# Kernel tuning notes

Measured on AMD Instinct MI355X. Metric: run time of the kernel, lower is better.

The kernel has to match this reference:

```python
import jax, jax.numpy as jnp
import numpy as np

B, T, H = 4, 2048, 1024
DFF = 4 * H
MAX_DEPTH = 4
TARGET_DEPTH = 2.5
BUDGET_WEIGHT = 0.01
ACT_TAU = 0.99


def setup_inputs() -> dict:
    key = jax.random.key(0)
    ks = jax.random.split(key, 6)
    s = 0.02
    return {
        "x": jax.random.normal(ks[0], (B, T, H), dtype=jnp.float32),
        "Wb1": jax.random.normal(ks[1], (H, DFF), dtype=jnp.float32) * s,
        "bb1": jnp.zeros((DFF,), dtype=jnp.float32),
        "Wb2": jax.random.normal(ks[2], (DFF, H), dtype=jnp.float32) * s,
        "bb2": jnp.zeros((H,), dtype=jnp.float32),
        "Rw1": jax.random.normal(ks[3], (MAX_DEPTH - 1, H + 1, H // 2), dtype=jnp.float32) * s,
        "Rb1": jnp.zeros((MAX_DEPTH - 1, H // 2), dtype=jnp.float32),
        "Rw2": jax.random.normal(ks[4], (MAX_DEPTH - 1, H // 2, 1), dtype=jnp.float32) * s,
        "Rb2": jnp.zeros((MAX_DEPTH - 1, 1), dtype=jnp.float32),
    }


def _body(x, Wb1, bb1, Wb2, bb2):
    # transformer-style FFN body, exact (erf) GELU to match torch nn.GELU
    h = jax.nn.gelu(jnp.einsum("btd,df->btf", x, Wb1) + bb1, approximate=False)
    return jnp.einsum("btf,fd->btd", h, Wb2) + bb2


def reference(x, Wb1, bb1, Wb2, bb2, Rw1, Rb1, Rw2, Rb2):
    # mandatory first pass
    x = _body(x, Wb1, bb1, Wb2, bb2)
    lead = x.shape[:-1]  # (B, T)
    weight_sum = jnp.ones(lead, dtype=x.dtype)
    cumulative_p = jnp.zeros(lead, dtype=x.dtype)
    still_running = jnp.ones(lead, dtype=x.dtype)
    for i in range(MAX_DEPTH - 1):
        # router: concat spike-rate feature (zeros: no scalar aux from body)
        feat = jnp.concatenate([x, jnp.zeros(lead + (1,), dtype=x.dtype)], axis=-1)
        h = jax.nn.gelu(jnp.einsum("btf,fm->btm", feat, Rw1[i]) + Rb1[i], approximate=False)
        logit = (jnp.einsum("btm,mo->bto", h, Rw2[i]) + Rb2[i])[..., 0]
        p = jax.nn.sigmoid(logit)
        # ACT remainder trick
        remainder = jnp.clip(1.0 - cumulative_p, 0.0)
        would_halt = cumulative_p + p >= ACT_TAU
        weight = jnp.where(would_halt, remainder, p) * still_running
        # soft depth mix
        x_new = _body(x, Wb1, bb1, Wb2, bb2)
        w = weight[..., None]
        x = w * x_new + (1.0 - w) * x
        weight_sum = weight_sum + weight
        cumulative_p = cumulative_p + weight
        still_running = still_running * (~would_halt).astype(x.dtype)
    avg_depth = weight_sum.mean()
    budget_loss = BUDGET_WEIGHT * jnp.square(jax.nn.relu(avg_depth - TARGET_DEPTH))
    return x, budget_loss
```

## Files before the change

kernel.cpp:

```cpp
#include <hip/hip_runtime.h>
#include <hip/hip_bf16.h>
#include <math.h>

typedef __bf16 bf16_t;
typedef __attribute__((ext_vector_type(8))) __bf16 bf16x8;
typedef __attribute__((ext_vector_type(4))) __bf16 bf16x4;
typedef __attribute__((ext_vector_type(4))) float f32x4;

#define NTOK 8192
#define HDIM 1024
#define DFF  4096
#define RHID 512

__device__ __forceinline__ float gelu_exact(float v) {
  return 0.5f * v * (1.0f + erff(v * 0.70710678118654752f));
}

__device__ __forceinline__ void async_cp16(void* lds, const void* g) {
  __builtin_amdgcn_global_load_lds(
      (__attribute__((address_space(1))) void*)g,
      (__attribute__((address_space(3))) void*)lds, 16, 0, 0);
}

__device__ __forceinline__ void remap_tile(int g, int& mt, int& nt) {
  mt = ((g & 7) << 3) | ((g >> 3) & 7);
  nt = g >> 6;
}

template<int MODE>
__device__ __forceinline__ void body_tile(
    int mt, int nt,
    const bf16_t* __restrict__ A, const bf16_t* __restrict__ Bt,
    const float* __restrict__ bias, int N, int K,
    bf16_t* __restrict__ Hout, float* __restrict__ Xout,
    bf16_t* __restrict__ Xb, bf16_t* __restrict__ Xlo,
    const float* __restrict__ Wmix,
    bf16_t* As, bf16_t* Bs)
{
  const int tid  = threadIdx.x;
  const int lane = tid & 63;
  const int wv   = tid >> 6;
  const int wm   = wv >> 1;
  const int wn   = wv & 1;
  const int lr   = lane & 15;
  const int quad = lane >> 4;
  const int m0 = mt * 128;
  const int n0 = nt * 128;

  f32x4 acc[4][4];
#pragma unroll
  for (int i = 0; i < 4; ++i)
#pragma unroll
    for (int j = 0; j < 4; ++j)
      acc[i][j] = (f32x4){0.f, 0.f, 0.f, 0.f};

  const int c0 = tid;
  const int c1 = tid + 256;
  const int r0 = c0 >> 2, r1 = c1 >> 2;
  const int ks0 = ((c0 ^ r0) & 3) * 8;
  const int ks1 = ((c1 ^ r1) & 3) * 8;
  const bf16_t* Ag0 = A  + (size_t)(m0 + r0) * K + ks0;
  const bf16_t* Ag1 = A  + (size_t)(m0 + r1) * K + ks1;
  const bf16_t* Bg0 = Bt + (size_t)(n0 + r0) * K + ks0;
  const bf16_t* Bg1 = Bt + (size_t)(n0 + r1) * K + ks1;
  char* lA0 = (char*)As + c0 * 16;
  char* lA1 = (char*)As + c1 * 16;
  char* lB0 = (char*)Bs + c0 * 16;
  char* lB1 = (char*)Bs + c1 * 16;

  const int sw = ((quad ^ lr) & 3) * 8;

  for (int k0 = 0; k0 < K; k0 += 32) {
    __syncthreads();
    async_cp16(lA0, Ag0 + k0);
    async_cp16(lA1, Ag1 + k0);
    async_cp16(lB0, Bg0 + k0);
    async_cp16(lB1, Bg1 + k0);
    __syncthreads();
    bf16x8 af[4], bfr[4];
#pragma unroll
    for (int i = 0; i < 4; ++i)
      af[i] = *(const bf16x8*)&As[(wm * 64 + i * 16 + lr) * 32 + sw];
#pragma unroll
    for (int j = 0; j < 4; ++j)
      bfr[j] = *(const bf16x8*)&Bs[(wn * 64 + j * 16 + lr) * 32 + sw];
#pragma unroll
    for (int i = 0; i < 4; ++i)
#pragma unroll
      for (int j = 0; j < 4; ++j)
        acc[i][j] = __builtin_amdgcn_mfma_f32_16x16x32_bf16(af[i], bfr[j], acc[i][j], 0, 0, 0);
  }

#pragma unroll
  for (int i = 0; i < 4; ++i) {
#pragma unroll
    for (int r = 0; r < 4; ++r) {
      const int gm = m0 + wm * 64 + i * 16 + quad * 4 + r;
      float wmix = 0.f, onemw = 0.f;
      if (MODE == 2) { wmix = Wmix[gm]; onemw = 1.f - wmix; }
#pragma unroll
      for (int j = 0; j < 4; ++j) {
        const int gn = n0 + wn * 64 + j * 16 + lr;
        float v = acc[i][j][r] + bias[gn];
        if (MODE == 0) {
          Hout[(size_t)gm * N + gn] = (bf16_t)gelu_exact(v);
        } else {
          const size_t idx = (size_t)gm * N + gn;
          if (MODE == 2) v = wmix * v + onemw * Xout[idx];
          Xout[idx] = v;
          bf16_t hi = (bf16_t)v;
          Xb[idx]  = hi;
          Xlo[idx] = (bf16_t)(v - (float)hi);
        }
      }
    }
  }
}

__device__ __forceinline__ void router_tile(
    int mt, int nt,
    const bf16_t* __restrict__ Ah, const bf16_t* __restrict__ Al,
    const bf16_t* __restrict__ Bh, const bf16_t* __restrict__ Bl,
    const float* __restrict__ bias, float* __restrict__ Hr,
    bf16_t* Ahs, bf16_t* Als, bf16_t* Bhs, bf16_t* Bls)
{
  const int K = HDIM, N = RHID;
  const int tid  = threadIdx.x;
  const int lane = tid & 63;
  const int wv   = tid >> 6;
  const int wm   = wv >> 1;
  const int wn   = wv & 1;
  const int lr   = lane & 15;
  const int quad = lane >> 4;
  const int m0 = mt * 128;
  const int n0 = nt * 128;

  f32x4 acc[4][4];
#pragma unroll
  for (int i = 0; i < 4; ++i)
#pragma unroll
    for (int j = 0; j < 4; ++j)
      acc[i][j] = (f32x4){0.f, 0.f, 0.f, 0.f};

  const int c0 = tid;
  const int c1 = tid + 256;
  const int r0 = c0 >> 2, r1 = c1 >> 2;
  const int ks0 = ((c0 ^ r0) & 3) * 8;
  const int ks1 = ((c1 ^ r1) & 3) * 8;
  const size_t aoff0 = (size_t)(m0 + r0) * K + ks0;
  const size_t aoff1 = (size_t)(m0 + r1) * K + ks1;
  const size_t boff0 = (size_t)(n0 + r0) * K + ks0;
  const size_t boff1 = (size_t)(n0 + r1) * K + ks1;
  const int sw = ((quad ^ lr) & 3) * 8;

  for (int k0 = 0; k0 < K; k0 += 32) {
    __syncthreads();
    async_cp16((char*)Ahs + c0 * 16, Ah + aoff0 + k0);
    async_cp16((char*)Ahs + c1 * 16, Ah + aoff1 + k0);
    async_cp16((char*)Als + c0 * 16, Al + aoff0 + k0);
    async_cp16((char*)Als + c1 * 16, Al + aoff1 + k0);
    async_cp16((char*)Bhs + c0 * 16, Bh + boff0 + k0);
    async_cp16((char*)Bhs + c1 * 16, Bh + boff1 + k0);
    async_cp16((char*)Bls + c0 * 16, Bl + boff0 + k0);
    async_cp16((char*)Bls + c1 * 16, Bl + boff1 + k0);
    __syncthreads();
    bf16x8 ah[4], al[4], bh[4], bl[4];
#pragma unroll
    for (int i = 0; i < 4; ++i) {
      const int ao = (wm * 64 + i * 16 + lr) * 32 + sw;
      ah[i] = *(const bf16x8*)&Ahs[ao];
      al[i] = *(const bf16x8*)&Als[ao];
    }
#pragma unroll
    for (int j = 0; j < 4; ++j) {
      const int bo = (wn * 64 + j * 16 + lr) * 32 + sw;
      bh[j] = *(const bf16x8*)&Bhs[bo];
      bl[j] = *(const bf16x8*)&Bls[bo];
    }
#pragma unroll
    for (int i = 0; i < 4; ++i)
#pragma unroll
      for (int j = 0; j < 4; ++j) {
        acc[i][j] = __builtin_amdgcn_mfma_f32_16x16x32_bf16(ah[i], bh[j], acc[i][j], 0, 0, 0);
        acc[i][j] = __builtin_amdgcn_mfma_f32_16x16x32_bf16(al[i], bh[j], acc[i][j], 0, 0, 0);
        acc[i][j] = __builtin_amdgcn_mfma_f32_16x16x32_bf16(ah[i], bl[j], acc[i][j], 0, 0, 0);
      }
  }

#pragma unroll
  for (int i = 0; i < 4; ++i)
#pragma unroll
    for (int r = 0; r < 4; ++r) {
      const int gm = m0 + wm * 64 + i * 16 + quad * 4 + r;
#pragma unroll
      for (int j = 0; j < 4; ++j) {
        const int gn = n0 + wn * 64 + j * 16 + lr;
        Hr[(size_t)gm * N + gn] = gelu_exact(acc[i][j][r] + bias[gn]);
      }
    }
}

template<int MODE>
__global__ __launch_bounds__(256, 2)
void k_gemm(const bf16_t* __restrict__ A, const bf16_t* __restrict__ Bt,
            const float* __restrict__ bias, int N, int K,
            float* __restrict__ Xout, bf16_t* __restrict__ Xb,
            bf16_t* __restrict__ Xlo, const float* __restrict__ Wmix)
{
  __shared__ __align__(16) bf16_t sm[2 * 128 * 32];
  int mt, nt;
  remap_tile(blockIdx.x, mt, nt);
  body_tile<MODE>(mt, nt, A, Bt, bias, N, K, nullptr, Xout, Xb, Xlo, Wmix,
                  sm, sm + 128 * 32);
}

__global__ __launch_bounds__(256, 2)
void k_body0_router(const bf16_t* __restrict__ xb, const bf16_t* __restrict__ W1t,
                    const float* __restrict__ bb1, bf16_t* __restrict__ hbuf,
                    const bf16_t* __restrict__ xlo,
                    const bf16_t* __restrict__ R1h, const bf16_t* __restrict__ R1l,
                    const float* __restrict__ Rb1, float* __restrict__ hr,
                    int nbody)
{
  __shared__ __align__(16) bf16_t sm[4 * 128 * 32];
  const int g = blockIdx.x;
  if (g < nbody) {
    int mt, nt;
    remap_tile(g, mt, nt);
    body_tile<0>(mt, nt, xb, W1t, bb1, DFF, HDIM, hbuf,
                 nullptr, nullptr, nullptr, nullptr, sm, sm + 128 * 32);
  } else {
    int mt, nt;
    remap_tile(g - nbody, mt, nt);
    router_tile(mt, nt, xb, xlo, R1h, R1l, Rb1, hr,
                sm, sm + 128 * 32, sm + 2 * 128 * 32, sm + 3 * 128 * 32);
  }
}

__global__ void act_kernel(const float* __restrict__ Hr,
                           const float* __restrict__ rw2, const float* __restrict__ rb2,
                           float* __restrict__ cum_p, float* __restrict__ still_r,
                           float* __restrict__ wsum, float* __restrict__ wvec)
{
  const int t = blockIdx.x * 4 + (threadIdx.x >> 6);
  const int lane = threadIdx.x & 63;
  float s = 0.f;
#pragma unroll
  for (int j = 0; j < 8; ++j) {
    const int m = lane + j * 64;
    s += Hr[(size_t)t * RHID + m] * rw2[m];
  }
  for (int off = 32; off > 0; off >>= 1) s += __shfl_down(s, off, 64);
  if (lane == 0) {
    const float logit = s + rb2[0];
    const float p = 1.f / (1.f + expf(-logit));
    const float cum = cum_p[t];
    const float still = still_r[t];
    const float rem = fmaxf(1.f - cum, 0.f);
    const bool halt = (cum + p) >= 0.99f;
    const float w = (halt ? rem : p) * still;
    wvec[t] = w;
    wsum[t] += w;
    cum_p[t] = cum + w;
    if (halt) still_r[t] = 0.f;
  }
}

__global__ void transpose_to_bf16(const float* __restrict__ src, int srcld, int dstld,
                                  bf16_t* __restrict__ dst, bf16_t* __restrict__ dlo)
{
  __shared__ float tile[32][33];
  const int tx = threadIdx.x & 31;
  const int ty = threadIdx.x >> 5;
  const int bx = blockIdx.x;
  const int by = blockIdx.y;
#pragma unroll
  for (int l = 0; l < 4; ++l)
    tile[ty + l * 8][tx] = src[(size_t)(by * 32 + ty + l * 8) * srcld + bx * 32 + tx];
  __syncthreads();
#pragma unroll
  for (int l = 0; l < 4; ++l) {
    const int c = bx * 32 + ty + l * 8;
    const int r = by * 32 + tx;
    const float v = tile[tx][ty + l * 8];
    const bf16_t hi = (bf16_t)v;
    dst[(size_t)c * dstld + r] = hi;
    if (dlo) dlo[(size_t)c * dstld + r] = (bf16_t)(v - (float)hi);
  }
}

__global__ void cvt_x_kernel(const float4* __restrict__ x, bf16x4* __restrict__ xb, int n4)
{
  const int i = blockIdx.x * 256 + threadIdx.x;
  if (i >= n4) return;
  const float4 v = x[i];
  bf16x4 hb;
  hb[0] = (bf16_t)v.x; hb[1] = (bf16_t)v.y; hb[2] = (bf16_t)v.z; hb[3] = (bf16_t)v.w;
  xb[i] = hb;
}

__global__ void init_state_kernel(float* __restrict__ cum, float* __restrict__ still,
                                  float* __restrict__ wsum)
{
  const int i = blockIdx.x * 256 + threadIdx.x;
  cum[i] = 0.f; still[i] = 1.f; wsum[i] = 1.f;
}

__global__ void finalize_kernel(const float* __restrict__ wsum, float* __restrict__ out)
{
  __shared__ float red[256];
  float s = 0.f;
  for (int i = threadIdx.x; i < NTOK; i += 256) s += wsum[i];
  red[threadIdx.x] = s;
  __syncthreads();
  for (int o = 128; o > 0; o >>= 1) {
    if (threadIdx.x < o) red[threadIdx.x] += red[threadIdx.x + o];
    __syncthreads();
  }
  if (threadIdx.x == 0) {
    const float avg = red[0] / (float)NTOK;
    float d = avg - 2.5f;
    d = fmaxf(d, 0.f);
    out[0] = 0.01f * d * d;
  }
}

extern "C" void kernel_launch(void* const* d_in, const int* in_sizes, int n_in,
                              void* d_out, int out_size, void* d_ws, size_t ws_size,
                              hipStream_t stream) {
  const float* x   = (const float*)d_in[0];
  const float* Wb1 = (const float*)d_in[1];
  const float* bb1 = (const float*)d_in[2];
  const float* Wb2 = (const float*)d_in[3];
  const float* bb2 = (const float*)d_in[4];
  const float* Rw1 = (const float*)d_in[5];
  const float* Rb1 = (const float*)d_in[6];
  const float* Rw2 = (const float*)d_in[7];
  const float* Rb2 = (const float*)d_in[8];
  float* out = (float*)d_out;

  char* ws = (char*)d_ws;
  size_t off = 0;
  auto carve = [&](size_t bytes) -> void* {
    void* p = ws + off;
    off += (bytes + 255) & ~(size_t)255;
    return p;
  };
  bf16_t* xb   = (bf16_t*)carve((size_t)NTOK * HDIM * 2);
  bf16_t* xlo  = (bf16_t*)carve((size_t)NTOK * HDIM * 2);
  bf16_t* hbuf = (bf16_t*)carve((size_t)NTOK * DFF * 2);
  bf16_t* W1t  = (bf16_t*)carve((size_t)HDIM * DFF * 2);
  bf16_t* W2t  = (bf16_t*)carve((size_t)HDIM * DFF * 2);
  bf16_t* R1h  = (bf16_t*)carve((size_t)3 * RHID * HDIM * 2);
  bf16_t* R1l  = (bf16_t*)carve((size_t)3 * RHID * HDIM * 2);
  float*  hr   = (float*)carve((size_t)NTOK * RHID * 4);
  float*  cum  = (float*)carve((size_t)NTOK * 4);
  float*  stil = (float*)carve((size_t)NTOK * 4);
  float*  wsum = (float*)carve((size_t)NTOK * 4);
  float*  wvec = (float*)carve((size_t)NTOK * 4);

  transpose_to_bf16<<<dim3(128, 32), 256, 0, stream>>>(Wb1, DFF, HDIM, W1t, nullptr);
  transpose_to_bf16<<<dim3(32, 128), 256, 0, stream>>>(Wb2, HDIM, DFF, W2t, nullptr);
  for (int i = 0; i < 3; ++i)
    transpose_to_bf16<<<dim3(16, 32), 256, 0, stream>>>(
        Rw1 + (size_t)i * 1025 * RHID, RHID, HDIM,
        R1h + (size_t)i * RHID * HDIM, R1l + (size_t)i * RHID * HDIM);
  cvt_x_kernel<<<8192, 256, 0, stream>>>((const float4*)x, (bf16x4*)xb, NTOK * HDIM / 4);
  init_state_kernel<<<32, 256, 0, stream>>>(cum, stil, wsum);

  k_body0_router<<<2048, 256, 0, stream>>>(xb, W1t, bb1, hbuf, xlo,
                                           nullptr, nullptr, nullptr, nullptr, 2048);
  k_gemm<1><<<512, 256, 0, stream>>>(hbuf, W2t, bb2, HDIM, DFF, out, xb, xlo, nullptr);

  for (int i = 0; i < 3; ++i) {
    k_body0_router<<<2048 + 256, 256, 0, stream>>>(
        xb, W1t, bb1, hbuf, xlo,
        R1h + (size_t)i * RHID * HDIM, R1l + (size_t)i * RHID * HDIM,
        Rb1 + (size_t)i * RHID, hr, 2048);
    act_kernel<<<2048, 256, 0, stream>>>(hr, Rw2 + (size_t)i * RHID, Rb2 + i,
                                         cum, stil, wsum, wvec);
    k_gemm<2><<<512, 256, 0, stream>>>(hbuf, W2t, bb2, HDIM, DFF, out, xb, xlo, wvec);
  }

  finalize_kernel<<<1, 256, 0, stream>>>(wsum, out + (size_t)NTOK * HDIM);
  (void)in_sizes; (void)n_in; (void)out_size; (void)ws_size;
}
```

Before: 994.1 us.

## Double-buffer GEMM LDS loads and drop redundant fp32 x writes

The body GEMM main loop now double-buffers its LDS tiles. The next K-slice is issued by async global-to-LDS copy before computing on the current one, and one of the two barriers per iteration is removed. The mixing epilogue rebuilds the old x from the bf16 hi/lo pair instead of reading the fp32 output, and the fp32 output is written only on the final depth step. This cuts epilogue global traffic. The cost is doubled LDS usage per block, which may affect occupancy with the router path that shares the kernel.

```diff
diff --git a/kernel.cpp b/kernel.cpp
--- a/kernel.cpp
+++ b/kernel.cpp
@@ -27,7 +27,7 @@
   nt = g >> 6;
 }
 
-template<int MODE>
+template<int MODE, bool WRITE_OUT>
 __device__ __forceinline__ void body_tile(
     int mt, int nt,
     const bf16_t* __restrict__ A, const bf16_t* __restrict__ Bt,
@@ -69,21 +69,33 @@
   char* lB1 = (char*)Bs + c1 * 16;
 
   const int sw = ((quad ^ lr) & 3) * 8;
-
-  for (int k0 = 0; k0 < K; k0 += 32) {
+  const int KB = K >> 5;
+
+  async_cp16(lA0, Ag0);
+  async_cp16(lA1, Ag1);
+  async_cp16(lB0, Bg0);
+  async_cp16(lB1, Bg1);
+
+  for (int kb = 0; kb < KB; ++kb) {
     __syncthreads();
-    async_cp16(lA0, Ag0 + k0);
-    async_cp16(lA1, Ag1 + k0);
-    async_cp16(lB0, Bg0 + k0);
-    async_cp16(lB1, Bg1 + k0);
-    __syncthreads();
+    const int cur = kb & 1;
+    if (kb + 1 < KB) {
+      const int nb = (1 - cur) * 8192;
+      const int ko = (kb + 1) << 5;
+      async_cp16(lA0 + nb, Ag0 + ko);
+      async_cp16(lA1 + nb, Ag1 + ko);
+      async_cp16(lB0 + nb, Bg0 + ko);
+      async_cp16(lB1 + nb, Bg1 + ko);
+    }
+    const bf16_t* Asc = As + cur * 4096;
+    const bf16_t* Bsc = Bs + cur * 4096;
     bf16x8 af[4], bfr[4];
 #pragma unroll
     for (int i = 0; i < 4; ++i)
-      af[i] = *(const bf16x8*)&As[(wm * 64 + i * 16 + lr) * 32 + sw];
+      af[i] = *(const bf16x8*)&Asc[(wm * 64 + i * 16 + lr) * 32 + sw];
 #pragma unroll
     for (int j = 0; j < 4; ++j)
-      bfr[j] = *(const bf16x8*)&Bs[(wn * 64 + j * 16 + lr) * 32 + sw];
+      bfr[j] = *(const bf16x8*)&Bsc[(wn * 64 + j * 16 + lr) * 32 + sw];
 #pragma unroll
     for (int i = 0; i < 4; ++i)
 #pragma unroll
@@ -106,11 +118,14 @@
           Hout[(size_t)gm * N + gn] = (bf16_t)gelu_exact(v);
         } else {
           const size_t idx = (size_t)gm * N + gn;
-          if (MODE == 2) v = wmix * v + onemw * Xout[idx];
-          Xout[idx] = v;
-          bf16_t hi = (bf16_t)v;
+          if (MODE == 2) {
+            const float xold = (float)Xb[idx] + (float)Xlo[idx];
+            v = wmix * v + onemw * xold;
+          }
+          const bf16_t hi = (bf16_t)v;
           Xb[idx]  = hi;
           Xlo[idx] = (bf16_t)(v - (float)hi);
+          if (WRITE_OUT) Xout[idx] = v;
         }
       }
     }
@@ -200,18 +215,18 @@
     }
 }
 
-template<int MODE>
+template<int MODE, bool WRITE_OUT>
 __global__ __launch_bounds__(256, 2)
 void k_gemm(const bf16_t* __restrict__ A, const bf16_t* __restrict__ Bt,
             const float* __restrict__ bias, int N, int K,
             float* __restrict__ Xout, bf16_t* __restrict__ Xb,
             bf16_t* __restrict__ Xlo, const float* __restrict__ Wmix)
 {
-  __shared__ __align__(16) bf16_t sm[2 * 128 * 32];
+  __shared__ __align__(16) bf16_t sm[4 * 128 * 32];
   int mt, nt;
   remap_tile(blockIdx.x, mt, nt);
-  body_tile<MODE>(mt, nt, A, Bt, bias, N, K, nullptr, Xout, Xb, Xlo, Wmix,
-                  sm, sm + 128 * 32);
+  body_tile<MODE, WRITE_OUT>(mt, nt, A, Bt, bias, N, K, nullptr, Xout, Xb, Xlo, Wmix,
+                             sm, sm + 2 * 128 * 32);
 }
 
 __global__ __launch_bounds__(256, 2)
@@ -227,8 +242,9 @@
   if (g < nbody) {
     int mt, nt;
     remap_tile(g, mt, nt);
-    body_tile<0>(mt, nt, xb, W1t, bb1, DFF, HDIM, hbuf,
-                 nullptr, nullptr, nullptr, nullptr, sm, sm + 128 * 32);
+    body_tile<0, false>(mt, nt, xb, W1t, bb1, DFF, HDIM, hbuf,
+                        nullptr, nullptr, nullptr, nullptr,
+                        sm, sm + 2 * 128 * 32);
   } else {
     int mt, nt;
     remap_tile(g - nbody, mt, nt);
@@ -370,7 +386,8 @@
 
   k_body0_router<<<2048, 256, 0, stream>>>(xb, W1t, bb1, hbuf, xlo,
                                            nullptr, nullptr, nullptr, nullptr, 2048);
-  k_gemm<1><<<512, 256, 0, stream>>>(hbuf, W2t, bb2, HDIM, DFF, out, xb, xlo, nullptr);
+  k_gemm<1, false><<<512, 256, 0, stream>>>(hbuf, W2t, bb2, HDIM, DFF,
+                                            nullptr, xb, xlo, nullptr);
 
   for (int i = 0; i < 3; ++i) {
     k_body0_router<<<2048 + 256, 256, 0, stream>>>(
@@ -379,7 +396,12 @@
         Rb1 + (size_t)i * RHID, hr, 2048);
     act_kernel<<<2048, 256, 0, stream>>>(hr, Rw2 + (size_t)i * RHID, Rb2 + i,
                                          cum, stil, wsum, wvec);
-    k_gemm<2><<<512, 256, 0, stream>>>(hbuf, W2t, bb2, HDIM, DFF, out, xb, xlo, wvec);
+    if (i < 2)
+      k_gemm<2, false><<<512, 256, 0, stream>>>(hbuf, W2t, bb2, HDIM, DFF,
+                                                nullptr, xb, xlo, wvec);
+    else
+      k_gemm<2, true><<<512, 256, 0, stream>>>(hbuf, W2t, bb2, HDIM, DFF,
+                                               out, xb, xlo, wvec);
   }
 
   finalize_kernel<<<1, 256, 0, stream>>>(wsum, out + (size_t)NTOK * HDIM);
```

Result: faster. 931.7 us (-6.3%).
